# Kernel tuning notes

Measured on AMD Instinct MI355X. Metric: run time of the kernel, lower is better.

The kernel has to match this reference:

```python
import jax, jax.numpy as jnp
import numpy as np

EMBED_DIM = 1024
NUM_HEADS = 16
HEAD_DIM = EMBED_DIM // NUM_HEADS
SCALE = HEAD_DIM ** -0.5


def setup_inputs() -> dict:
    key = jax.random.key(0)
    ks = jax.random.split(key, 5)
    B, N, C = 4, 2048, EMBED_DIM
    s = C ** -0.5
    return {
        "x": jax.random.normal(ks[0], (B, N, C), dtype=jnp.float32),
        "w_qkv": jax.random.normal(ks[1], (C, 3 * C), dtype=jnp.float32) * s,
        "b_qkv": jnp.zeros((3 * C,), dtype=jnp.float32),
        "w_proj": jax.random.normal(ks[2], (C, C), dtype=jnp.float32) * s,
        "b_proj": jnp.zeros((C,), dtype=jnp.float32),
    }


def reference(x, w_qkv, b_qkv, w_proj, b_proj):
    B, N, C = x.shape
    H, D = NUM_HEADS, HEAD_DIM
    qkv = x @ w_qkv + b_qkv                      # (B, N, 3C)
    qkv = qkv.reshape(B, N, 3, H, D)
    qkv = jnp.transpose(qkv, (2, 0, 3, 1, 4))    # (3, B, H, N, D)
    q, k, v = qkv[0], qkv[1], qkv[2]
    attn = jnp.einsum('bhnd,bhmd->bhnm', q, k) * SCALE
    attn = jax.nn.softmax(attn, axis=-1)
    out = jnp.einsum('bhnm,bhmd->bhnd', attn, v)  # (B, H, N, D)
    out = jnp.transpose(out, (0, 2, 1, 3)).reshape(B, N, C)
    return out @ w_proj + b_proj
```

## Files before the change

kernel.cpp:

```cpp
#include <hip/hip_runtime.h>

typedef __attribute__((ext_vector_type(8))) short short8v;
typedef __attribute__((ext_vector_type(4))) short short4v;
typedef __attribute__((ext_vector_type(4))) float float4v;
typedef __attribute__((ext_vector_type(4))) unsigned short ushort4v;
typedef __attribute__((ext_vector_type(8))) unsigned short ushort8v;

#define GLOBAL_AS __attribute__((address_space(1)))
#define LDS_AS __attribute__((address_space(3)))

__device__ __forceinline__ void async_cp16(const void* g, void* l) {
  __builtin_amdgcn_global_load_lds((const GLOBAL_AS void*)g, (LDS_AS void*)l, 16, 0, 0);
}

__device__ __forceinline__ unsigned short f2bf(float f) {
  unsigned u = __float_as_uint(f);
  u += 0x7fffu + ((u >> 16) & 1u);
  return (unsigned short)(u >> 16);
}

#if defined(__HIP_DEVICE_COMPILE__)
#if __has_builtin(__builtin_amdgcn_exp2f)
#define EXP2F(x) __builtin_amdgcn_exp2f(x)
#else
#define EXP2F(x) exp2f(x)
#endif
#else
#define EXP2F(x) exp2f(x)
#endif

#if defined(__HIP_DEVICE_COMPILE__) && __has_builtin(__builtin_amdgcn_cvt_pk_bf16_f32)
typedef __attribute__((ext_vector_type(2))) __bf16 bf16x2v;
__device__ __forceinline__ unsigned pk_bf16(float a, float b) {
  bf16x2v r = __builtin_amdgcn_cvt_pk_bf16_f32(a, b);
  return __builtin_bit_cast(unsigned, r);
}
#else
__device__ __forceinline__ unsigned pk_bf16(float a, float b) {
  return (unsigned)f2bf(a) | ((unsigned)f2bf(b) << 16);
}
#endif

#define MFMA_QK(a, b, c) __builtin_amdgcn_mfma_f32_16x16x32_bf16(a, b, c, 0, 0, 0)

__device__ __forceinline__ void wg_barrier() {
  asm volatile("" ::: "memory");
  __builtin_amdgcn_s_barrier();
  asm volatile("" ::: "memory");
}


__global__ __launch_bounds__(256) void cvt_f32_bf16(const float* __restrict__ src,
                                                    unsigned short* __restrict__ dst) {
  int i = blockIdx.x * 256 + threadIdx.x;
  float4 v = ((const float4*)src)[i];
  ushort4v o;
  o.x = f2bf(v.x); o.y = f2bf(v.y); o.z = f2bf(v.z); o.w = f2bf(v.w);
  ((ushort4v*)dst)[i] = o;
}

__global__ __launch_bounds__(256) void transpose_w(const float* __restrict__ src,
                                                   unsigned short* __restrict__ dst,
                                                   int K, int N) {
  __shared__ float tile[64][65];
  int k0 = blockIdx.x * 64, n0 = blockIdx.y * 64;
  int t = threadIdx.x;
  int tc = t & 15, tr = t >> 4;
#pragma unroll
  for (int p = 0; p < 4; p++) {
    int r = tr + p * 16;
    float4 v = *(const float4*)(src + (size_t)(k0 + r) * N + n0 + tc * 4);
    tile[r][tc * 4 + 0] = v.x; tile[r][tc * 4 + 1] = v.y;
    tile[r][tc * 4 + 2] = v.z; tile[r][tc * 4 + 3] = v.w;
  }
  __syncthreads();
#pragma unroll
  for (int p = 0; p < 4; p++) {
    int rn = tr + p * 16;
    ushort4v o;
    o.x = f2bf(tile[tc * 4 + 0][rn]);
    o.y = f2bf(tile[tc * 4 + 1][rn]);
    o.z = f2bf(tile[tc * 4 + 2][rn]);
    o.w = f2bf(tile[tc * 4 + 3][rn]);
    *(ushort4v*)(dst + (size_t)(n0 + rn) * K + k0 + tc * 4) = o;
  }
}

__device__ __forceinline__ void stage128x32(const unsigned short* __restrict__ src,
                                            unsigned short* dst, int r0, int k0, int tid) {
#pragma unroll
  for (int p = 0; p < 2; p++) {
    int idx = p * 256 + tid;
    int row = idx >> 2, s = idx & 3;
    int ch = s ^ ((row >> 1) & 3);
    async_cp16(src + (size_t)(r0 + row) * 1024 + k0 + ch * 8, dst + idx * 8);
  }
}


#define TT_STRIDE 136

__global__ __launch_bounds__(256) void gemm_qkv(const unsigned short* __restrict__ A,
                                                const unsigned short* __restrict__ BT,
                                                const float* __restrict__ bias,
                                                unsigned short* __restrict__ Qo,
                                                unsigned short* __restrict__ Ko,
                                                unsigned short* __restrict__ VTo) {
  __shared__ unsigned short smem[24576];
  int tid = threadIdx.x;
  int lane = tid & 63, w = tid >> 6, g = lane >> 4, c = lane & 15;
  int m0 = blockIdx.x * 128, n0 = blockIdx.y * 128;
  int wm = (w & 1) * 64, wn = (w >> 1) * 64;
  float4v acc[4][4] = {};

  stage128x32(A, smem + 0 * 4096, m0, 0, tid);
  stage128x32(BT, smem + 12288 + 0 * 4096, n0, 0, tid);
  stage128x32(A, smem + 1 * 4096, m0, 32, tid);
  stage128x32(BT, smem + 12288 + 1 * 4096, n0, 32, tid);
  asm volatile("s_waitcnt vmcnt(4)" ::: "memory");
  wg_barrier();

  int cb = 0;
  for (int t = 0; t < 32; ++t) {
    int nb = cb + 2; if (nb >= 3) nb -= 3;
    const unsigned short* Ap = smem + cb * 4096;
    const unsigned short* Bp = smem + 12288 + cb * 4096;

    short8v af[4], bf[4];
#pragma unroll
    for (int i = 0; i < 4; i++) {
      int r = wm + i * 16 + c;
      af[i] = *(const short8v*)(Ap + r * 32 + (g ^ ((r >> 1) & 3)) * 8);
    }
#pragma unroll
    for (int j = 0; j < 4; j++) {
      int r = wn + j * 16 + c;
      bf[j] = *(const short8v*)(Bp + r * 32 + (g ^ ((r >> 1) & 3)) * 8);
    }

    if (t + 2 < 32) {
      stage128x32(A, smem + nb * 4096, m0, (t + 2) * 32, tid);
      stage128x32(BT, smem + 12288 + nb * 4096, n0, (t + 2) * 32, tid);
    }

    __builtin_amdgcn_s_setprio(1);
#pragma unroll
    for (int i = 0; i < 4; i++)
#pragma unroll
      for (int j = 0; j < 4; j++)
        acc[i][j] = MFMA_QK(af[i], bf[j], acc[i][j]);
    __builtin_amdgcn_s_setprio(0);

    if (t < 30) { asm volatile("s_waitcnt vmcnt(4)" ::: "memory"); }
    else        { asm volatile("s_waitcnt vmcnt(0)" ::: "memory"); }
    wg_barrier();
    cb = cb + 1 == 3 ? 0 : cb + 1;
  }

  int which = n0 >> 10;
  if (which != 2) {
#pragma unroll
    for (int j = 0; j < 4; j++) {
      int ng = n0 + wn + j * 16 + c;
      float bv = bias[ng];
      int h = (ng & 1023) >> 6, d = ng & 63;
#pragma unroll
      for (int i = 0; i < 4; i++) {
#pragma unroll
        for (int r = 0; r < 4; r++) {
          int mg = m0 + wm + i * 16 + g * 4 + r;
          int b = mg >> 11, n = mg & 2047;
          float v = acc[i][j][r] + bv;
          if (which == 0)
            Qo[((size_t)(b * 16 + h) * 2048 + n) * 64 + d] = f2bf(v * 0.18033688011112042f);
          else
            Ko[((size_t)(b * 16 + h) * 2048 + n) * 64 + d] = f2bf(v);
        }
      }
    }
  } else {
    __syncthreads();
#pragma unroll
    for (int j = 0; j < 4; j++) {
      int nl = wn + j * 16 + c;
      float bv = bias[n0 + nl];
#pragma unroll
      for (int i = 0; i < 4; i++) {
        int ml = wm + i * 16 + g * 4;
        unsigned p0 = pk_bf16(acc[i][j][0] + bv, acc[i][j][1] + bv);
        unsigned p1 = pk_bf16(acc[i][j][2] + bv, acc[i][j][3] + bv);
        *(unsigned*)(smem + nl * TT_STRIDE + ml) = p0;
        *(unsigned*)(smem + nl * TT_STRIDE + ml + 2) = p1;
      }
    }
    __syncthreads();
    int rr = lane >> 4, tc = lane & 15;
    int P = tc & 3, g32 = tc >> 2;
    int b = m0 >> 11, mloc = m0 & 2047;
    int h0 = (n0 & 1023) >> 6;
#pragma unroll
    for (int s = 0; s < 8; s++) {
      int row = w * 32 + s * 4 + rr;
      int h = h0 + (row >> 6), d = row & 63;
      const unsigned short* bp = smem + row * TT_STRIDE + g32 * 32 + P * 4;
      union { unsigned long long q[2]; ushort8v v; } u;
      u.q[0] = *(const unsigned long long*)(bp);
      u.q[1] = *(const unsigned long long*)(bp + 16);
      size_t gaddr = ((size_t)(b * 16 + h) * 64 + d) * 2048 + mloc + g32 * 32 + P * 8;
      *(ushort8v*)(VTo + gaddr) = u.v;
    }
  }
}


#define NTOK 2048
#define BK 64

__device__ __forceinline__ short8v exppack(float4v a, float4v b2) {
  a.x = EXP2F(a.x); a.y = EXP2F(a.y); a.z = EXP2F(a.z); a.w = EXP2F(a.w);
  b2.x = EXP2F(b2.x); b2.y = EXP2F(b2.y); b2.z = EXP2F(b2.z); b2.w = EXP2F(b2.w);
  union { unsigned u[4]; short8v s; } cv;
  cv.u[0] = pk_bf16(a.x, a.y);
  cv.u[1] = pk_bf16(a.z, a.w);
  cv.u[2] = pk_bf16(b2.x, b2.y);
  cv.u[3] = pk_bf16(b2.z, b2.w);
  return cv.s;
}

__global__ __launch_bounds__(256, 4) void attn_kernel(const unsigned short* __restrict__ Qg,
                                                      const unsigned short* __restrict__ Kg,
                                                      const unsigned short* __restrict__ VTg,
                                                      unsigned short* __restrict__ Og) {
  __shared__ unsigned short Ks[2][BK * 64];

  int tid = threadIdx.x;
  int lane = tid & 63, w = tid >> 6, g = lane >> 4, c = lane & 15;
  int id = blockIdx.x;
  int xcd = id & 7, within = id >> 3;
  int bh = xcd * 8 + (within >> 4);
  int q0 = (within & 15) * 128;

  const unsigned short* Qb = Qg + (size_t)bh * NTOK * 64;
  const unsigned short* Kb = Kg + (size_t)bh * NTOK * 64;
  const unsigned short* VTb = VTg + (size_t)bh * 64 * NTOK;

  short8v qf[2][2];
#pragma unroll
  for (int nt = 0; nt < 2; nt++)
#pragma unroll
    for (int kk = 0; kk < 2; kk++)
      qf[nt][kk] = *(const short8v*)(Qb + (size_t)(q0 + w * 32 + nt * 16 + c) * 64 +
                                     kk * 32 + g * 8);

  short8v ones8;
#pragma unroll
  for (int i = 0; i < 8; i++) ones8[i] = (short)0x3F80;

  float4v lacc[2] = {};
  float4v o[2][4] = {};

  const unsigned short* vbase = VTb + (size_t)c * 2048 + g * 8;

#pragma unroll
  for (int p = 0; p < 2; p++) {
    int idx = p * 256 + tid;
    int row = idx >> 3, ch = idx & 7;
    async_cp16(Kb + (size_t)row * 64 + ((ch ^ (row & 7)) * 8), &Ks[0][idx * 8]);
  }

  for (int it = 0; it < NTOK / BK; it++) {
    int pb = it & 1;
    __syncthreads();

    if (it + 1 < NTOK / BK) {
      int kt = (it + 1) * BK;
#pragma unroll
      for (int p = 0; p < 2; p++) {
        int idx = p * 256 + tid;
        int row = idx >> 3, ch = idx & 7;
        async_cp16(Kb + (size_t)(kt + row) * 64 + ((ch ^ (row & 7)) * 8),
                   &Ks[1 - pb][idx * 8]);
      }
    }

    const unsigned short* Kp = &Ks[pb][0];

#pragma unroll
    for (int t = 0; t < 2; t++) {
      int ch32 = it * 2 + t;
      short8v vb[4];
#pragma unroll
      for (int nt_o = 0; nt_o < 4; nt_o++)
        vb[nt_o] = *(const short8v*)(vbase + (size_t)nt_o * 32768 + ch32 * 32);

      float4v st[2][2] = {};
      __builtin_amdgcn_s_setprio(1);
#pragma unroll
      for (int mth = 0; mth < 2; mth++) {
        int row = (t * 2 + mth) * 16 + c;
        short8v kf[2];
#pragma unroll
        for (int kk = 0; kk < 2; kk++) {
          int ch = (kk * 4 + g) ^ (row & 7);
          kf[kk] = *(const short8v*)(Kp + row * 64 + ch * 8);
        }
#pragma unroll
        for (int nt = 0; nt < 2; nt++)
#pragma unroll
          for (int kk = 0; kk < 2; kk++)
            st[mth][nt] = MFMA_QK(kf[kk], qf[nt][kk], st[mth][nt]);
      }
      __builtin_amdgcn_s_setprio(0);

      short8v pa8[2];
#pragma unroll
      for (int nt = 0; nt < 2; nt++) pa8[nt] = exppack(st[0][nt], st[1][nt]);

      __builtin_amdgcn_s_setprio(1);
#pragma unroll
      for (int nt_o = 0; nt_o < 4; nt_o++)
#pragma unroll
        for (int mt = 0; mt < 2; mt++)
          o[mt][nt_o] = MFMA_QK(pa8[mt], vb[nt_o], o[mt][nt_o]);
#pragma unroll
      for (int mt = 0; mt < 2; mt++)
        lacc[mt] = MFMA_QK(pa8[mt], ones8, lacc[mt]);
      __builtin_amdgcn_s_setprio(0);
    }
  }

  int b = bh >> 4, h = bh & 15;
#pragma unroll
  for (int mt = 0; mt < 2; mt++) {
    float4v li;
#pragma unroll
    for (int r = 0; r < 4; r++) li[r] = 1.0f / lacc[mt][r];
#pragma unroll
    for (int nt_o = 0; nt_o < 4; nt_o++) {
      float4v v = o[mt][nt_o] * li;
      int col = h * 64 + nt_o * 16 + c;
      int rowbase = b * NTOK + q0 + w * 32 + mt * 16 + g * 4;
#pragma unroll
      for (int r = 0; r < 4; r++)
        Og[(size_t)(rowbase + r) * 1024 + col] = f2bf(v[r]);
    }
  }
}

__global__ __launch_bounds__(256) void gemm_proj(const unsigned short* __restrict__ A,
                                                 const unsigned short* __restrict__ BT,
                                                 const float* __restrict__ bias,
                                                 float* __restrict__ out) {
  __shared__ unsigned short smem[24576];
  int tid = threadIdx.x;
  int lane = tid & 63, w = tid >> 6, g = lane >> 4, c = lane & 15;
  int m0 = blockIdx.x * 128, n0 = blockIdx.y * 128;
  int wm = (w & 1) * 64, wn = (w >> 1) * 64;
  float4v acc[4][4] = {};

  stage128x32(A, smem + 0 * 4096, m0, 0, tid);
  stage128x32(BT, smem + 12288 + 0 * 4096, n0, 0, tid);
  stage128x32(A, smem + 1 * 4096, m0, 32, tid);
  stage128x32(BT, smem + 12288 + 1 * 4096, n0, 32, tid);
  asm volatile("s_waitcnt vmcnt(4)" ::: "memory");
  wg_barrier();

  int cb = 0;
  for (int t = 0; t < 32; ++t) {
    int nb = cb + 2; if (nb >= 3) nb -= 3;
    const unsigned short* Ap = smem + cb * 4096;
    const unsigned short* Bp = smem + 12288 + cb * 4096;

    short8v af[4], bf[4];
#pragma unroll
    for (int i = 0; i < 4; i++) {
      int r = wm + i * 16 + c;
      af[i] = *(const short8v*)(Ap + r * 32 + (g ^ ((r >> 1) & 3)) * 8);
    }
#pragma unroll
    for (int j = 0; j < 4; j++) {
      int r = wn + j * 16 + c;
      bf[j] = *(const short8v*)(Bp + r * 32 + (g ^ ((r >> 1) & 3)) * 8);
    }

    if (t + 2 < 32) {
      stage128x32(A, smem + nb * 4096, m0, (t + 2) * 32, tid);
      stage128x32(BT, smem + 12288 + nb * 4096, n0, (t + 2) * 32, tid);
    }

    __builtin_amdgcn_s_setprio(1);
#pragma unroll
    for (int i = 0; i < 4; i++)
#pragma unroll
      for (int j = 0; j < 4; j++)
        acc[i][j] = MFMA_QK(af[i], bf[j], acc[i][j]);
    __builtin_amdgcn_s_setprio(0);

    if (t < 30) { asm volatile("s_waitcnt vmcnt(4)" ::: "memory"); }
    else        { asm volatile("s_waitcnt vmcnt(0)" ::: "memory"); }
    wg_barrier();
    cb = cb + 1 == 3 ? 0 : cb + 1;
  }

#pragma unroll
  for (int j = 0; j < 4; j++) {
    int ng = n0 + wn + j * 16 + c;
    float bv = bias[ng];
#pragma unroll
    for (int i = 0; i < 4; i++) {
#pragma unroll
      for (int r = 0; r < 4; r++) {
        int mg = m0 + wm + i * 16 + g * 4 + r;
        out[(size_t)mg * 1024 + ng] = acc[i][j][r] + bv;
      }
    }
  }
}


extern "C" void kernel_launch(void* const* d_in, const int* in_sizes, int n_in,
                              void* d_out, int out_size, void* d_ws, size_t ws_size,
                              hipStream_t stream) {
  (void)in_sizes; (void)n_in; (void)out_size; (void)ws_size;
  const float* x = (const float*)d_in[0];
  const float* w_qkv = (const float*)d_in[1];
  const float* b_qkv = (const float*)d_in[2];
  const float* w_proj = (const float*)d_in[3];
  const float* b_proj = (const float*)d_in[4];
  float* out = (float*)d_out;

  unsigned short* x_bf = (unsigned short*)d_ws;
  unsigned short* wqkvT = x_bf + (size_t)8192 * 1024;
  unsigned short* wprojT = wqkvT + (size_t)3072 * 1024;
  unsigned short* qws = wprojT + (size_t)1024 * 1024;
  unsigned short* kws = qws + (size_t)8388608;
  unsigned short* vtws = kws + (size_t)8388608;
  unsigned short* aws = vtws + (size_t)8388608;

  cvt_f32_bf16<<<8192, 256, 0, stream>>>(x, x_bf);
  transpose_w<<<dim3(16, 48), 256, 0, stream>>>(w_qkv, wqkvT, 1024, 3072);
  transpose_w<<<dim3(16, 16), 256, 0, stream>>>(w_proj, wprojT, 1024, 1024);
  gemm_qkv<<<dim3(64, 24), 256, 0, stream>>>(x_bf, wqkvT, b_qkv, qws, kws, vtws);
  attn_kernel<<<1024, 256, 0, stream>>>(qws, kws, vtws, aws);
  gemm_proj<<<dim3(64, 8), 256, 0, stream>>>(aws, wprojT, b_proj, out);
}
```

Baseline: 311.7 us.

## Give each attention wave its own LDS K/V pipeline with 64 query rows

The attention kernel now gives each wave 64 query rows instead of 32 and launches half as many blocks, so each loaded K/V chunk is reused across more queries. Each wave double-buffers its own K and V^T chunks in a private LDS region using async global-to-LDS copies, with swizzled layouts. Synchronisation is per wave through vmcnt waits rather than block-wide barriers. V is now staged through LDS instead of being read straight from global memory. This cuts block syncs and global traffic at the cost of more registers, 64KB of LDS per block and lower occupancy (launch bounds drop from 4 to 2).

```diff
diff --git a/kernel.cpp b/kernel.cpp
--- a/kernel.cpp
+++ b/kernel.cpp
@@ -214,7 +214,6 @@
 
 
 #define NTOK 2048
-#define BK 64
 
 __device__ __forceinline__ short8v exppack(float4v a, float4v b2) {
   a.x = EXP2F(a.x); a.y = EXP2F(a.y); a.z = EXP2F(a.z); a.w = EXP2F(a.w);
@@ -227,111 +226,117 @@
   return cv.s;
 }
 
-__global__ __launch_bounds__(256, 4) void attn_kernel(const unsigned short* __restrict__ Qg,
+__global__ __launch_bounds__(256, 2) void attn_kernel(const unsigned short* __restrict__ Qg,
                                                       const unsigned short* __restrict__ Kg,
                                                       const unsigned short* __restrict__ VTg,
                                                       unsigned short* __restrict__ Og) {
-  __shared__ unsigned short Ks[2][BK * 64];
+  __shared__ unsigned short smem[32768];
 
   int tid = threadIdx.x;
   int lane = tid & 63, w = tid >> 6, g = lane >> 4, c = lane & 15;
   int id = blockIdx.x;
   int xcd = id & 7, within = id >> 3;
-  int bh = xcd * 8 + (within >> 4);
-  int q0 = (within & 15) * 128;
+  int bh = xcd * 8 + (within >> 3);
+  int q0 = (within & 7) * 256;
 
   const unsigned short* Qb = Qg + (size_t)bh * NTOK * 64;
   const unsigned short* Kb = Kg + (size_t)bh * NTOK * 64;
   const unsigned short* VTb = VTg + (size_t)bh * 64 * NTOK;
 
-  short8v qf[2][2];
-#pragma unroll
-  for (int nt = 0; nt < 2; nt++)
+  unsigned short* wbase = smem + w * 8192;
+
+  short8v qf[4][2];
+#pragma unroll
+  for (int nt = 0; nt < 4; nt++)
 #pragma unroll
     for (int kk = 0; kk < 2; kk++)
-      qf[nt][kk] = *(const short8v*)(Qb + (size_t)(q0 + w * 32 + nt * 16 + c) * 64 +
+      qf[nt][kk] = *(const short8v*)(Qb + (size_t)(q0 + w * 64 + nt * 16 + c) * 64 +
                                      kk * 32 + g * 8);
 
   short8v ones8;
 #pragma unroll
   for (int i = 0; i < 8; i++) ones8[i] = (short)0x3F80;
 
-  float4v lacc[2] = {};
-  float4v o[2][4] = {};
-
-  const unsigned short* vbase = VTb + (size_t)c * 2048 + g * 8;
-
-#pragma unroll
-  for (int p = 0; p < 2; p++) {
-    int idx = p * 256 + tid;
-    int row = idx >> 3, ch = idx & 7;
-    async_cp16(Kb + (size_t)row * 64 + ((ch ^ (row & 7)) * 8), &Ks[0][idx * 8]);
-  }
-
-  for (int it = 0; it < NTOK / BK; it++) {
-    int pb = it & 1;
-    __syncthreads();
-
-    if (it + 1 < NTOK / BK) {
-      int kt = (it + 1) * BK;
-#pragma unroll
-      for (int p = 0; p < 2; p++) {
-        int idx = p * 256 + tid;
-        int row = idx >> 3, ch = idx & 7;
-        async_cp16(Kb + (size_t)(kt + row) * 64 + ((ch ^ (row & 7)) * 8),
-                   &Ks[1 - pb][idx * 8]);
+  float4v lacc[4] = {};
+  float4v o[4][4] = {};
+
+#define STAGE_CHUNK(pb_, ch32_)                                                   \
+  {                                                                               \
+    int kt_ = (ch32_) * 32;                                                       \
+    unsigned short* kd_ = wbase + (pb_) * 4096;                                   \
+    unsigned short* vd_ = kd_ + 2048;                                             \
+    _Pragma("unroll")                                                             \
+    for (int p_ = 0; p_ < 4; p_++) {                                              \
+      int u_ = p_ * 64 + lane;                                                    \
+      int row_ = u_ >> 3, sl_ = u_ & 7;                                           \
+      int ch_ = sl_ ^ (row_ & 7);                                                 \
+      async_cp16(Kb + (size_t)(kt_ + row_) * 64 + ch_ * 8, kd_ + u_ * 8);         \
+    }                                                                             \
+    _Pragma("unroll")                                                             \
+    for (int p_ = 0; p_ < 4; p_++) {                                              \
+      int u_ = p_ * 64 + lane;                                                    \
+      int d_ = u_ >> 2, s_ = u_ & 3;                                              \
+      int j_ = s_ ^ ((d_ & 2) ^ ((d_ >> 2) & 1));                                 \
+      async_cp16(VTb + (size_t)d_ * 2048 + kt_ + j_ * 8, vd_ + u_ * 8);           \
+    }                                                                             \
+  }
+
+  STAGE_CHUNK(0, 0)
+
+  for (int ch32 = 0; ch32 < 64; ch32++) {
+    int pb = ch32 & 1;
+    if (ch32 + 1 < 64) {
+      STAGE_CHUNK(1 - pb, ch32 + 1)
+      asm volatile("s_waitcnt vmcnt(8)" ::: "memory");
+    } else {
+      asm volatile("s_waitcnt vmcnt(0)" ::: "memory");
+    }
+
+    const unsigned short* Kp = wbase + pb * 4096;
+    const unsigned short* Vp = Kp + 2048;
+
+    float4v st[2][4] = {};
+    __builtin_amdgcn_s_setprio(1);
+#pragma unroll
+    for (int mth = 0; mth < 2; mth++) {
+      int row = mth * 16 + c;
+      short8v kf[2];
+#pragma unroll
+      for (int kk = 0; kk < 2; kk++) {
+        int sl = (kk * 4 + g) ^ (row & 7);
+        kf[kk] = *(const short8v*)(Kp + row * 64 + sl * 8);
       }
-    }
-
-    const unsigned short* Kp = &Ks[pb][0];
-
-#pragma unroll
-    for (int t = 0; t < 2; t++) {
-      int ch32 = it * 2 + t;
-      short8v vb[4];
-#pragma unroll
-      for (int nt_o = 0; nt_o < 4; nt_o++)
-        vb[nt_o] = *(const short8v*)(vbase + (size_t)nt_o * 32768 + ch32 * 32);
-
-      float4v st[2][2] = {};
-      __builtin_amdgcn_s_setprio(1);
-#pragma unroll
-      for (int mth = 0; mth < 2; mth++) {
-        int row = (t * 2 + mth) * 16 + c;
-        short8v kf[2];
-#pragma unroll
-        for (int kk = 0; kk < 2; kk++) {
-          int ch = (kk * 4 + g) ^ (row & 7);
-          kf[kk] = *(const short8v*)(Kp + row * 64 + ch * 8);
-        }
-#pragma unroll
-        for (int nt = 0; nt < 2; nt++)
-#pragma unroll
-          for (int kk = 0; kk < 2; kk++)
-            st[mth][nt] = MFMA_QK(kf[kk], qf[nt][kk], st[mth][nt]);
-      }
-      __builtin_amdgcn_s_setprio(0);
-
-      short8v pa8[2];
-#pragma unroll
-      for (int nt = 0; nt < 2; nt++) pa8[nt] = exppack(st[0][nt], st[1][nt]);
-
-      __builtin_amdgcn_s_setprio(1);
-#pragma unroll
-      for (int nt_o = 0; nt_o < 4; nt_o++)
-#pragma unroll
-        for (int mt = 0; mt < 2; mt++)
-          o[mt][nt_o] = MFMA_QK(pa8[mt], vb[nt_o], o[mt][nt_o]);
-#pragma unroll
-      for (int mt = 0; mt < 2; mt++)
-        lacc[mt] = MFMA_QK(pa8[mt], ones8, lacc[mt]);
-      __builtin_amdgcn_s_setprio(0);
-    }
+#pragma unroll
+      for (int nt = 0; nt < 4; nt++)
+#pragma unroll
+        for (int kk = 0; kk < 2; kk++)
+          st[mth][nt] = MFMA_QK(kf[kk], qf[nt][kk], st[mth][nt]);
+    }
+    __builtin_amdgcn_s_setprio(0);
+
+    short8v pa8[4];
+#pragma unroll
+    for (int nt = 0; nt < 4; nt++) pa8[nt] = exppack(st[0][nt], st[1][nt]);
+
+    __builtin_amdgcn_s_setprio(1);
+#pragma unroll
+    for (int nt_o = 0; nt_o < 4; nt_o++) {
+      int d = nt_o * 16 + c;
+      int s = g ^ ((d & 2) ^ ((d >> 2) & 1));
+      short8v vb8 = *(const short8v*)(Vp + d * 32 + s * 8);
+#pragma unroll
+      for (int mt = 0; mt < 4; mt++)
+        o[mt][nt_o] = MFMA_QK(pa8[mt], vb8, o[mt][nt_o]);
+    }
+#pragma unroll
+    for (int mt = 0; mt < 4; mt++)
+      lacc[mt] = MFMA_QK(pa8[mt], ones8, lacc[mt]);
+    __builtin_amdgcn_s_setprio(0);
   }
 
   int b = bh >> 4, h = bh & 15;
 #pragma unroll
-  for (int mt = 0; mt < 2; mt++) {
+  for (int mt = 0; mt < 4; mt++) {
     float4v li;
 #pragma unroll
     for (int r = 0; r < 4; r++) li[r] = 1.0f / lacc[mt][r];
@@ -339,7 +344,7 @@
     for (int nt_o = 0; nt_o < 4; nt_o++) {
       float4v v = o[mt][nt_o] * li;
       int col = h * 64 + nt_o * 16 + c;
-      int rowbase = b * NTOK + q0 + w * 32 + mt * 16 + g * 4;
+      int rowbase = b * NTOK + q0 + w * 64 + mt * 16 + g * 4;
 #pragma unroll
       for (int r = 0; r < 4; r++)
         Og[(size_t)(rowbase + r) * 1024 + col] = f2bf(v[r]);
@@ -441,6 +446,6 @@
   transpose_w<<<dim3(16, 48), 256, 0, stream>>>(w_qkv, wqkvT, 1024, 3072);
   transpose_w<<<dim3(16, 16), 256, 0, stream>>>(w_proj, wprojT, 1024, 1024);
   gemm_qkv<<<dim3(64, 24), 256, 0, stream>>>(x_bf, wqkvT, b_qkv, qws, kws, vtws);
-  attn_kernel<<<1024, 256, 0, stream>>>(qws, kws, vtws, aws);
+  attn_kernel<<<512, 256, 0, stream>>>(qws, kws, vtws, aws);
   gemm_proj<<<dim3(64, 8), 256, 0, stream>>>(aws, wprojT, b_proj, out);
 }
```

Result: faster. 268.4 us (-13.9%).
